# Kernel optimization log

Measured on AMD Instinct MI355X. Metric: run time of the kernel, lower is better.

## Reference

```python
import jax, jax.numpy as jnp
import numpy as np

B, NG, C, H = 16, 1024, 768, 12
CAP = 16  # fixed routing capacity in gpu_pair (8 box slots from 0 up, 8 cls slots from 15 down)


def layernorm(x, g, b, eps=1e-5):
    m = x.mean(-1, keepdims=True)
    v = jnp.mean((x - m) ** 2, axis=-1, keepdims=True)
    return (x - m) * jax.lax.rsqrt(v + eps) * g + b


def setup_inputs() -> dict:
    key = jax.random.key(0)
    ks = jax.random.split(key, 8)
    s = 0.02
    return {
        "general_token": jax.random.normal(ks[0], (B, NG, C), jnp.float32),
        "cls_token": jax.random.normal(ks[1], (B, 1, C), jnp.float32),
        "box_token": jax.random.normal(ks[2], (B, 1, C), jnp.float32),
        "w_qkv": jax.random.normal(ks[3], (3 * C, C), jnp.float32) * s,
        "w_proj": jax.random.normal(ks[4], (C, C), jnp.float32) * s,
        "b_proj": jnp.zeros((C,), jnp.float32),
        "gamma1": jnp.ones((C,), jnp.float32),
        "beta1": jnp.zeros((C,), jnp.float32),
    }


def _route(sum_a, is_box):
    """On-device replication of gpu_pair's serial CPU loop for slots 0..15.

    Tokens are processed in descending sum_attn order; box-preferred tokens fill
    slots 0,1,2,..., cls-preferred tokens fill slots 15,14,13,.... Each category's
    writer per slot is unique; on a box/cls collision the later (larger sorted
    position) write wins, matching the serial loop's overwrite semantics. Slots
    never written stay 0 (np.zeros init). Wrapped-around writes (rank >= 16) land
    outside slots 0..15 in the original and are irrelevant to the output.
    """
    ng = sum_a.shape[0]
    perm = jnp.argsort(-sum_a)                      # descending sort
    ib = is_box[perm]
    ibi = ib.astype(jnp.int32)
    box_rank = jnp.cumsum(ibi) - ibi                # exclusive prefix count of box tokens
    cls_rank = jnp.cumsum(1 - ibi) - (1 - ibi)      # exclusive prefix count of cls tokens
    j = jnp.arange(ng, dtype=jnp.int32)
    box_pos = jnp.where(ib & (box_rank < CAP), box_rank, CAP)
    cls_pos = jnp.where((~ib) & (cls_rank < CAP), (CAP - 1) - cls_rank, CAP)
    empty = jnp.full((CAP,), -1, jnp.int32)
    box_j = empty.at[box_pos].set(j, mode='drop')   # unique writer per slot
    cls_j = empty.at[cls_pos].set(j, mode='drop')
    win = jnp.maximum(box_j, cls_j)
    return jnp.where(win >= 0, perm[jnp.maximum(win, 0)], 0)


def reference(general_token, cls_token, box_token, w_qkv, w_proj, b_proj, gamma1, beta1):
    # cat order in torch: cat(cls, cat(box, general)) -> [cls, box, general]
    cat = jnp.concatenate([cls_token, box_token, general_token], axis=1)  # [B,N,C]
    Bq, N, Cq = cat.shape
    hd = Cq // H
    x = layernorm(cat, gamma1, beta1)
    qkv = (x @ w_qkv.T).reshape(Bq, N, 3, H, hd).transpose(2, 0, 3, 1, 4)
    q, k, v = qkv[0], qkv[1], qkv[2]
    attn = jnp.einsum('bhnd,bhmd->bhnm', q, k) * (hd ** -0.5)
    # raw scores between cls<->box zeroed BEFORE softmax (not -inf)
    attn = attn.at[:, :, 0, 1].set(0.0).at[:, :, 1, 0].set(0.0)
    attn = jax.nn.softmax(attn, axis=-1)
    out = jnp.einsum('bhnm,bhmd->bhnd', attn, v).transpose(0, 2, 1, 3).reshape(Bq, N, Cq)
    out = out @ w_proj.T + b_proj
    cat = cat + out  # residual (drop_path identity in eval)
    cls_t, box_t, gen = cat[:, 0:1], cat[:, 1:2], cat[:, 2:]
    cls_attn = attn[:, :, 0, 2:].mean(axis=1)  # [B, N-2]
    box_attn = attn[:, :, 1, 2:].mean(axis=1)
    idx = jax.vmap(_route)(cls_attn + box_attn, box_attn > cls_attn)  # [B,16]
    gathered = jnp.take_along_axis(gen, idx[:, :, None], axis=1)      # [B,16,C]
    cls_task_token = jnp.concatenate([cls_t, gathered[:, 0:8]], axis=1)   # [B,9,C]
    box_task_token = jnp.concatenate([box_t, gathered[:, 8:16]], axis=1)  # [B,9,C]
    return cls_task_token, box_task_token
```

## Files before the change

### kernel.cpp

```cpp
#include <hip/hip_runtime.h>
#include <math.h>

namespace {

constexpr int Bn = 16;
constexpr int NG = 1024;
constexpr int Cc = 768;
constexpr int Hh = 12;
constexpr int HD = 64;
constexpr int Nn = 1026;
constexpr int NR = 18;
constexpr int NPK = 1152;
constexpr int NCH = 16;

typedef __attribute__((ext_vector_type(8))) short short8;
typedef __attribute__((ext_vector_type(4))) float f32x4;

__device__ inline unsigned short f2bf(float f) {
  unsigned u = __float_as_uint(f);
  unsigned r = u + 0x7FFFu + ((u >> 16) & 1u);
  return (unsigned short)(r >> 16);
}

__global__ __launch_bounds__(256) void k_ln(
    const float* __restrict__ gen, const float* __restrict__ cls,
    const float* __restrict__ box, const float* __restrict__ gamma,
    const float* __restrict__ beta, float* __restrict__ x,
    unsigned short* __restrict__ xbf) {
  int blk = blockIdx.x;
  int t = threadIdx.x;
  if (blk >= Bn * Nn) {
    constexpr int PERB = (NPK - Nn) * Cc / 2;
    int idx = (blk - Bn * Nn) * 256 + t;
    int total = Bn * PERB;
    for (int i = idx; i < total; i += 96 * 256) {
      int b = i / PERB, r = i % PERB;
      unsigned int* p = (unsigned int*)(xbf + ((size_t)b * NPK + Nn) * Cc);
      p[r] = 0u;
    }
    return;
  }
  int b = blk / Nn, n = blk % Nn;
  const float* src = (n == 0) ? cls + (size_t)b * Cc
                   : (n == 1) ? box + (size_t)b * Cc
                              : gen + ((size_t)b * NG + (n - 2)) * Cc;
  float v0 = src[t], v1 = src[t + 256], v2 = src[t + 512];
  __shared__ double red[8];
  double s = (double)v0 + (double)v1 + (double)v2;
  for (int o = 32; o > 0; o >>= 1) s += __shfl_down(s, o, 64);
  int wid = t >> 6, lid = t & 63;
  if (lid == 0) red[wid] = s;
  __syncthreads();
  if (t == 0) red[4] = (red[0] + red[1] + red[2] + red[3]) / Cc;
  __syncthreads();
  double mean = red[4];
  double d0 = (double)v0 - mean, d1 = (double)v1 - mean, d2 = (double)v2 - mean;
  double sq = d0 * d0 + d1 * d1 + d2 * d2;
  for (int o = 32; o > 0; o >>= 1) sq += __shfl_down(sq, o, 64);
  __syncthreads();
  if (lid == 0) red[wid] = sq;
  __syncthreads();
  if (t == 0) {
    double var = (red[0] + red[1] + red[2] + red[3]) / Cc;
    red[5] = 1.0 / sqrt(var + 1e-5);
  }
  __syncthreads();
  double rs = red[5];
  float* dst = x + ((size_t)b * Nn + n) * Cc;
  unsigned short* dbf = xbf + ((size_t)b * NPK + n) * Cc;
  float o0 = (float)(d0 * rs * (double)gamma[t]       + (double)beta[t]);
  float o1 = (float)(d1 * rs * (double)gamma[t + 256] + (double)beta[t + 256]);
  float o2 = (float)(d2 * rs * (double)gamma[t + 512] + (double)beta[t + 512]);
  dst[t] = o0; dst[t + 256] = o1; dst[t + 512] = o2;
  dbf[t] = f2bf(o0); dbf[t + 256] = f2bf(o1); dbf[t + 512] = f2bf(o2);
}

__global__ __launch_bounds__(256) void k_mega1(
    const unsigned short* __restrict__ xbf, unsigned short* __restrict__ xT,
    const float* __restrict__ wqkv, const float* __restrict__ wproj,
    unsigned short* __restrict__ wqb, unsigned short* __restrict__ wvb,
    unsigned short* __restrict__ wpb, unsigned short* __restrict__ wkTb,
    const float* __restrict__ x, double* __restrict__ q01d) {
  __shared__ __align__(16) char smem[64 * 80 * 2];
  int blk = blockIdx.x;
  int t = threadIdx.x;
  if (blk < 3456) {
    int b = blk / 216, rem = blk % 216;
    int jt = rem / 12, ct = rem % 12;
    int j0 = jt * 64, c0 = ct * 64;
    auto ts = (unsigned short(*)[80])smem;
    #pragma unroll
    for (int l = 0; l < 2; l++) {
      int chunk = t + l * 256;
      int r = chunk >> 3, c8 = chunk & 7;
      uint4 v = *(const uint4*)(xbf + ((size_t)b * NPK + j0 + r) * Cc + c0 + c8 * 8);
      *(uint4*)&ts[r][c8 * 8] = v;
    }
    __syncthreads();
    #pragma unroll
    for (int l = 0; l < 2; l++) {
      int chunk = t + l * 256;
      int orow = chunk >> 3, j8 = chunk & 7;
      unsigned short tmp[8];
      #pragma unroll
      for (int i = 0; i < 8; i++) tmp[i] = ts[j8 * 8 + i][orow];
      *(uint4*)(xT + ((size_t)b * Cc + c0 + orow) * NPK + j0 + j8 * 8) = *(uint4*)tmp;
    }
  } else if (blk < 4032) {
    int i = ((blk - 3456) * 256 + t) * 4;
    const float* wq = wqkv;
    const float* wv = wqkv + (size_t)2 * Cc * Cc;
    float4 q = *(const float4*)(wq + i);
    float4 a = *(const float4*)(wv + i);
    float4 b = *(const float4*)(wproj + i);
    ushort4 oq, oa, ob;
    oq.x = f2bf(q.x); oq.y = f2bf(q.y); oq.z = f2bf(q.z); oq.w = f2bf(q.w);
    oa.x = f2bf(a.x); oa.y = f2bf(a.y); oa.z = f2bf(a.z); oa.w = f2bf(a.w);
    ob.x = f2bf(b.x); ob.y = f2bf(b.y); ob.z = f2bf(b.z); ob.w = f2bf(b.w);
    *(ushort4*)(wqb + i) = oq;
    *(ushort4*)(wvb + i) = oa;
    *(ushort4*)(wpb + i) = ob;
  } else if (blk < 4176) {
    int q = blk - 4032;
    int rt = q / 12, ct = q % 12;
    auto ts = (unsigned short(*)[72])smem;
    const float* src = wqkv + (size_t)Cc * Cc;
    #pragma unroll
    for (int l = 0; l < 4; l++) {
      int idx = t + l * 256;
      int r = idx >> 4, c4 = idx & 15;
      float4 v = *(const float4*)(src + (size_t)(rt * 64 + r) * Cc + ct * 64 + c4 * 4);
      ts[r][c4 * 4 + 0] = f2bf(v.x); ts[r][c4 * 4 + 1] = f2bf(v.y);
      ts[r][c4 * 4 + 2] = f2bf(v.z); ts[r][c4 * 4 + 3] = f2bf(v.w);
    }
    __syncthreads();
    #pragma unroll
    for (int l = 0; l < 2; l++) {
      int idx = t + l * 256;
      int r2 = idx >> 3, j8 = idx & 7;
      unsigned short tmp[8];
      #pragma unroll
      for (int i = 0; i < 8; i++) tmp[i] = ts[j8 * 8 + i][r2];
      *(uint4*)(wkTb + (size_t)(ct * 64 + r2) * Cc + rt * 64 + j8 * 8) = *(uint4*)tmp;
    }
  } else {
    int q = blk - 4176;
    int row = q & 31;
    int ot = q >> 5;
    int b = row >> 1, i = row & 1;
    float* xl = (float*)smem;
    const float* xr = x + ((size_t)b * Nn + i) * Cc;
    for (int c = t; c < Cc; c += 256) xl[c] = xr[c];
    __syncthreads();
    int w = t >> 6, lane = t & 63;
    int o = ot * 4 + w;
    const float* wr = wqkv + (size_t)o * Cc + lane * 12;
    const float* xs = xl + lane * 12;
    double acc = 0;
    #pragma unroll
    for (int k = 0; k < 12; k++) acc += (double)wr[k] * (double)xs[k];
    for (int off = 32; off > 0; off >>= 1) acc += __shfl_down(acc, off, 64);
    if (lane == 0) q01d[(size_t)row * Cc + o] = acc;
  }
}

__global__ __launch_bounds__(256) void k_u01(
    const float* __restrict__ wqkv, const double* __restrict__ q01d,
    double* __restrict__ u01d) {
  int blk = blockIdx.x;
  int h = blk % Hh; int i = (blk / Hh) & 1; int b = blk / (2 * Hh);
  __shared__ double qh[HD];
  const double* q = q01d + ((size_t)b * 2 + i) * Cc + h * HD;
  if (threadIdx.x < HD) qh[threadIdx.x] = q[threadIdx.x];
  __syncthreads();
  const float* wk = wqkv + (size_t)Cc * Cc;
  int c = blockIdx.y * 256 + threadIdx.x;
  double a0 = 0, a1 = 0, a2 = 0, a3 = 0;
  #pragma unroll 4
  for (int d = 0; d < HD; d += 4) {
    a0 += qh[d]     * (double)wk[(size_t)(h * HD + d) * Cc + c];
    a1 += qh[d + 1] * (double)wk[(size_t)(h * HD + d + 1) * Cc + c];
    a2 += qh[d + 2] * (double)wk[(size_t)(h * HD + d + 2) * Cc + c];
    a3 += qh[d + 3] * (double)wk[(size_t)(h * HD + d + 3) * Cc + c];
  }
  u01d[(((size_t)(b * 2 + i)) * Hh + h) * Cc + c] = (a0 + a1) + (a2 + a3);
}

__global__ __launch_bounds__(256) void k_mega2(
    const double* __restrict__ u01d, const float* __restrict__ x,
    float* __restrict__ Ldp, double* __restrict__ Ld01) {
  int blk = blockIdx.x;
  int t = threadIdx.x;
  if (blk >= 1024) {
    int q = blk - 1024;
    int b = q >> 1, i = q & 1;
    int w = t >> 6, lane = t & 63;
    for (int k = 0; k < 6; k++) {
      int p = w * 6 + k;
      int h = p >> 1, j = p & 1;
      const double* u = u01d + (((size_t)(b * 2 + i)) * Hh + h) * Cc;
      const float* xr = x + ((size_t)b * Nn + j) * Cc;
      double acc = 0;
      for (int c = lane; c < Cc; c += 64) acc += u[c] * (double)xr[c];
      for (int off = 32; off > 0; off >>= 1) acc += __shfl_down(acc, off, 64);
      if (lane == 0) Ld01[(((size_t)(b * 2 + i)) * Hh + h) * 2 + j] = acc * 0.125;
    }
    return;
  }
  int b = blk >> 6, jt = (blk >> 4) & 3, cch = blk & 15;
  int c0 = cch * 48;
  int w = t >> 6, lane = t & 63;
  int g = w >> 1;
  int hh = (w & 1) * 6;
  __shared__ double ut[24][48];
  __shared__ __align__(16) float xtT[16][260];
  for (int idx = t; idx < 24 * 48; idx += 256) {
    int row = idx / 48, cc = idx % 48;
    int ig = row / 12, hr = row % 12;
    ut[row][cc] = u01d[(((size_t)(b * 2 + ig)) * Hh + hr) * Cc + c0 + cc];
  }
  double acc[6][4] = {};
  for (int s = 0; s < 3; s++) {
    #pragma unroll
    for (int l = 0; l < 4; l++) {
      int idx = t + l * 256;
      int row = idx >> 2, c4 = idx & 3;
      const float* xr = x + ((size_t)b * Nn + 2 + jt * 256 + row) * Cc + c0 + s * 16 + c4 * 4;
      float4 v = *(const float4*)xr;
      xtT[c4 * 4 + 0][row] = v.x;
      xtT[c4 * 4 + 1][row] = v.y;
      xtT[c4 * 4 + 2][row] = v.z;
      xtT[c4 * 4 + 3][row] = v.w;
    }
    __syncthreads();
    for (int cc = 0; cc < 16; cc++) {
      float4 xa = *(const float4*)&xtT[cc][lane * 4];
      double x0 = (double)xa.x, x1 = (double)xa.y, x2 = (double)xa.z, x3 = (double)xa.w;
      #pragma unroll
      for (int r = 0; r < 6; r++) {
        double uv = ut[g * 12 + hh + r][s * 16 + cc];
        acc[r][0] += uv * x0; acc[r][1] += uv * x1;
        acc[r][2] += uv * x2; acc[r][3] += uv * x3;
      }
    }
    __syncthreads();
  }
  for (int r = 0; r < 6; r++) {
    int rowo = g * 12 + hh + r;
    float4 o0;
    o0.x = (float)(acc[r][0] * 0.125); o0.y = (float)(acc[r][1] * 0.125);
    o0.z = (float)(acc[r][2] * 0.125); o0.w = (float)(acc[r][3] * 0.125);
    size_t base = (((size_t)cch * Bn + b) * 24 + rowo) * 1024 + jt * 256 + lane * 4;
    *(float4*)&Ldp[base] = o0;
  }
}

__global__ __launch_bounds__(256) void k_rsoftmax(
    const float* __restrict__ Ldp, const double* __restrict__ Ld01,
    double* __restrict__ Ld, unsigned short* __restrict__ Pb) {
  int blk = blockIdx.x;
  int h = blk % Hh; int i = (blk / Hh) & 1; int b = blk / (2 * Hh);
  double* row = Ld + (size_t)blk * Nn;
  unsigned short* prow = Pb + ((size_t)b * 216 + i * Hh + h) * NPK;
  int t = threadIdx.x;
  size_t poff = ((size_t)b * 24 + i * 12 + h) * 1024;
  constexpr size_t PSTRIDE = (size_t)Bn * 24 * 1024;
  double lv[5];
  int cnt = 0;
  double mx = -1e300;
  for (int j = t; j < Nn; j += 256) {
    double L;
    if (j < 2) {
      L = Ld01[(((size_t)(b * 2 + i)) * Hh + h) * 2 + j];
      if (i == 0 && j == 1) L = 0.0;
      if (i == 1 && j == 0) L = 0.0;
    } else {
      L = 0;
      #pragma unroll
      for (int p = 0; p < NCH; p++) L += (double)Ldp[(size_t)p * PSTRIDE + poff + (j - 2)];
    }
    lv[cnt++] = L;
    mx = fmax(mx, L);
  }
  __shared__ double sd[256];
  sd[t] = mx; __syncthreads();
  for (int st = 128; st > 0; st >>= 1) { if (t < st) sd[t] = fmax(sd[t], sd[t + st]); __syncthreads(); }
  mx = sd[0]; __syncthreads();
  double sum = 0;
  for (int k = 0; k < cnt; k++) { lv[k] = exp(lv[k] - mx); sum += lv[k]; }
  sd[t] = sum; __syncthreads();
  for (int st = 128; st > 0; st >>= 1) { if (t < st) sd[t] += sd[t + st]; __syncthreads(); }
  double inv = 1.0 / sd[0];
  int k = 0;
  for (int j = t; j < Nn; j += 256) {
    double p = lv[k++] * inv;
    row[j] = p;
    prow[j] = f2bf((float)p);
  }
  for (int j = Nn + t; j < NPK; j += 256) prow[j] = 0;
}

__global__ __launch_bounds__(256) void k_rsroute(
    const double* __restrict__ Ld, int* __restrict__ rowcat) {
  int b = blockIdx.x, t = threadIdx.x;
  __shared__ double vals[NG];
  __shared__ unsigned char flags[NG];
  __shared__ double redv[4];
  __shared__ int redi[4];
  __shared__ int blist[16], clist[16];
  __shared__ double blv[16], clv[16];
  for (int jg = t; jg < NG; jg += 256) {
    int j = jg + 2;
    double cs = 0, bs = 0;
    for (int h = 0; h < Hh; h++) {
      cs += Ld[(((size_t)(b * 2 + 0)) * Hh + h) * Nn + j];
      bs += Ld[(((size_t)(b * 2 + 1)) * Hh + h) * Nn + j];
    }
    cs /= 12.0; bs /= 12.0;
    vals[jg] = cs + bs;
    flags[jg] = (bs - cs) > 0.0 ? 1 : 0;
  }
  __syncthreads();
  int half = t >> 7;
  int lt = t & 127;
  int wv = t >> 6;
  int lane = t & 63;
  for (int s = 0; s < 16; s++) {
    double bv = -1e300; int bi = 0x7fffffff;
    #pragma unroll
    for (int k = 0; k < 8; k++) {
      int j = lt * 8 + k;
      double v = vals[j];
      if (flags[j] == half && v > bv) { bv = v; bi = j; }
    }
    for (int off = 32; off > 0; off >>= 1) {
      double ov = __shfl_down(bv, off, 64);
      int oi = __shfl_down(bi, off, 64);
      if (ov > bv || (ov == bv && oi < bi)) { bv = ov; bi = oi; }
    }
    if (lane == 0) { redv[wv] = bv; redi[wv] = bi; }
    __syncthreads();
    if (lt == 0) {
      double v0 = redv[half * 2], v1 = redv[half * 2 + 1];
      int i0 = redi[half * 2], i1 = redi[half * 2 + 1];
      if (v1 > v0 || (v1 == v0 && i1 < i0)) { v0 = v1; i0 = i1; }
      int win = (v0 > -1e299) ? i0 : -1;
      if (half) { blist[s] = win; blv[s] = v0; }
      else      { clist[s] = win; clv[s] = v0; }
      if (win >= 0) vals[win] = -1e300;
    }
    __syncthreads();
  }
  if (t < 16) {
    int s = t;
    int bc = blist[s];
    int cl = clist[15 - s];
    double bvv = blv[s], cvv = clv[15 - s];
    int win;
    if (bc < 0 && cl < 0) win = -1;
    else if (bc < 0) win = cl;
    else if (cl < 0) win = bc;
    else {
      bool boxwins = (bvv < cvv) || (bvv == cvv && bc > cl);
      win = boxwins ? bc : cl;
    }
    int tok = (win >= 0) ? win : 0;
    rowcat[b * NR + 2 + s] = tok + 2;
  }
  if (t == 0) { rowcat[b * NR + 0] = 0; rowcat[b * NR + 1] = 1; }
}

__global__ __launch_bounds__(256) void k_qg_mfma(
    const unsigned short* __restrict__ xbf, const unsigned short* __restrict__ wqb,
    const int* __restrict__ rowcat, unsigned short* __restrict__ qb) {
  int mt = blockIdx.x, ng = blockIdx.y;
  int wid = threadIdx.x >> 6, lane = threadIdx.x & 63;
  int nt = ng * 4 + wid;
  int m = lane & 15, kg = lane >> 4;
  int rowi = mt * 16 + m;
  int b = rowi >> 4, s = rowi & 15;
  int tok = rowcat[b * NR + 2 + s];
  const unsigned short* abase = xbf + ((size_t)b * NPK + tok) * Cc + kg * 8;
  const unsigned short* bbase = wqb + (size_t)(nt * 16 + m) * Cc + kg * 8;
  f32x4 acc = {0, 0, 0, 0};
  for (int k0 = 0; k0 < Cc; k0 += 32) {
    short8 a = *(const short8*)(abase + k0);
    short8 bf = *(const short8*)(bbase + k0);
    acc = __builtin_amdgcn_mfma_f32_16x16x32_bf16(a, bf, acc, 0, 0, 0);
  }
  int c = nt * 16 + m;
  #pragma unroll
  for (int r = 0; r < 4; r++) {
    int rowo = mt * 16 + kg * 4 + r;
    qb[(size_t)rowo * Cc + c] = f2bf(acc[r]);
  }
}

__global__ __launch_bounds__(256) void k_ug_mfma(
    const unsigned short* __restrict__ qb, const unsigned short* __restrict__ wkTb,
    unsigned short* __restrict__ u16b) {
  int h = blockIdx.x, mt = blockIdx.y, ngz = blockIdx.z;
  int wid = threadIdx.x >> 6, lane = threadIdx.x & 63;
  int m = lane & 15, kg = lane >> 4;
  int rowi = mt * 16 + m;
  const unsigned short* abase = qb + (size_t)rowi * Cc + h * HD + kg * 8;
  f32x4 acc[4] = {{0,0,0,0},{0,0,0,0},{0,0,0,0},{0,0,0,0}};
  #pragma unroll
  for (int k0 = 0; k0 < HD; k0 += 32) {
    short8 a = *(const short8*)(abase + k0);
    #pragma unroll
    for (int t = 0; t < 4; t++) {
      int c = ngz * 256 + (wid * 4 + t) * 16 + m;
      short8 bf = *(const short8*)(wkTb + (size_t)c * Cc + h * HD + kg * 8 + k0);
      acc[t] = __builtin_amdgcn_mfma_f32_16x16x32_bf16(a, bf, acc[t], 0, 0, 0);
    }
  }
  #pragma unroll
  for (int t = 0; t < 4; t++) {
    int c = ngz * 256 + (wid * 4 + t) * 16 + m;
    #pragma unroll
    for (int r = 0; r < 4; r++) {
      int row = mt * 16 + kg * 4 + r;
      int b = row >> 4, s = row & 15;
      u16b[((size_t)b * 192 + s * Hh + h) * Cc + c] = f2bf(acc[t][r]);
    }
  }
}

__global__ __launch_bounds__(128) void k_glogits_mfma(
    const unsigned short* __restrict__ u16b, const unsigned short* __restrict__ xbf,
    float* __restrict__ S) {
  int b = blockIdx.x, mg = blockIdx.y, nz = blockIdx.z;
  __shared__ __align__(16) unsigned short Bs[2][128 * 32];
  int t = threadIdx.x, w = t >> 6, lane = t & 63;
  int m = lane & 15, kg = lane >> 4;
  const unsigned short* ap[4];
  #pragma unroll
  for (int mt = 0; mt < 4; mt++)
    ap[mt] = u16b + ((size_t)b * 192 + mg * 64 + mt * 16 + m) * Cc + kg * 8;
  const unsigned short* gB[4];
  int lofs[4];
  #pragma unroll
  for (int l = 0; l < 4; l++) {
    int chunk = l * 128 + t;
    int col = chunk >> 2, kq = chunk & 3;
    gB[l] = xbf + ((size_t)b * NPK + nz * 128 + col) * Cc + kq * 8;
    lofs[l] = col * 32 + kq * 8;
  }
  constexpr int NIT = Cc / 32;
  #pragma unroll
  for (int l = 0; l < 4; l++) *(short8*)&Bs[0][lofs[l]] = *(const short8*)gB[l];
  __syncthreads();
  f32x4 acc[4][4] = {};
  for (int it = 0; it < NIT; it++) {
    int k0 = it * 32;
    int cur = it & 1;
    short8 nx[4];
    if (it + 1 < NIT) {
      #pragma unroll
      for (int l = 0; l < 4; l++) nx[l] = *(const short8*)(gB[l] + k0 + 32);
    }
    short8 a[4];
    #pragma unroll
    for (int mt = 0; mt < 4; mt++) a[mt] = *(const short8*)(ap[mt] + k0);
    #pragma unroll
    for (int tt = 0; tt < 4; tt++) {
      int col = w * 64 + tt * 16 + m;
      short8 bf = *(const short8*)&Bs[cur][col * 32 + kg * 8];
      #pragma unroll
      for (int mt = 0; mt < 4; mt++)
        acc[mt][tt] = __builtin_amdgcn_mfma_f32_16x16x32_bf16(a[mt], bf, acc[mt][tt], 0, 0, 0);
    }
    if (it + 1 < NIT) {
      #pragma unroll
      for (int l = 0; l < 4; l++) *(short8*)&Bs[cur ^ 1][lofs[l]] = nx[l];
    }
    __syncthreads();
  }
  #pragma unroll
  for (int mt = 0; mt < 4; mt++) {
    #pragma unroll
    for (int tt = 0; tt < 4; tt++) {
      int col = nz * 128 + w * 64 + tt * 16 + m;
      #pragma unroll
      for (int r = 0; r < 4; r++) {
        int row = mg * 64 + mt * 16 + kg * 4 + r;
        S[((size_t)b * 192 + row) * NPK + col] = acc[mt][tt][r] * 0.125f;
      }
    }
  }
}

__global__ __launch_bounds__(256) void k_gsoftmax(
    const float* __restrict__ S, unsigned short* __restrict__ Pb) {
  int blk = blockIdx.x;
  int b = blk / 192, r = blk % 192;
  const float* row = S + ((size_t)b * 192 + r) * NPK;
  unsigned short* prow = Pb + ((size_t)b * 216 + 24 + r) * NPK;
  int t = threadIdx.x;
  __shared__ float sd[256];
  float mx = -1e30f;
  for (int j = t; j < Nn; j += 256) mx = fmaxf(mx, row[j]);
  sd[t] = mx; __syncthreads();
  for (int st = 128; st > 0; st >>= 1) { if (t < st) sd[t] = fmaxf(sd[t], sd[t + st]); __syncthreads(); }
  mx = sd[0]; __syncthreads();
  float sum = 0;
  for (int j = t; j < Nn; j += 256) sum += __expf(row[j] - mx);
  sd[t] = sum; __syncthreads();
  for (int st = 128; st > 0; st >>= 1) { if (t < st) sd[t] += sd[t + st]; __syncthreads(); }
  float inv = 1.0f / sd[0];
  for (int j = t; j < NPK; j += 256) {
    prow[j] = (j < Nn) ? f2bf(__expf(row[j] - mx) * inv) : (unsigned short)0;
  }
}

__global__ __launch_bounds__(128) void k_wsum_mfma(
    const unsigned short* __restrict__ Pb, const unsigned short* __restrict__ xT,
    unsigned short* __restrict__ wsumb) {
  int b = blockIdx.x, mg = blockIdx.y, nz = blockIdx.z;
  __shared__ __align__(16) unsigned short Bs[2][128 * 32];
  int t = threadIdx.x, w = t >> 6, lane = t & 63;
  int m = lane & 15, kg = lane >> 4;
  const unsigned short* ap[4];
  #pragma unroll
  for (int mt = 0; mt < 4; mt++) {
    int r = mg * 64 + mt * 16 + m;
    int rc = r < 216 ? r : 215;
    ap[mt] = Pb + ((size_t)b * 216 + rc) * NPK + kg * 8;
  }
  const unsigned short* gB[4];
  int lofs[4];
  #pragma unroll
  for (int l = 0; l < 4; l++) {
    int chunk = l * 128 + t;
    int col = chunk >> 2, kq = chunk & 3;
    gB[l] = xT + ((size_t)b * Cc + nz * 128 + col) * NPK + kq * 8;
    lofs[l] = col * 32 + kq * 8;
  }
  constexpr int NIT = NPK / 32;
  #pragma unroll
  for (int l = 0; l < 4; l++) *(short8*)&Bs[0][lofs[l]] = *(const short8*)gB[l];
  __syncthreads();
  f32x4 acc[4][4] = {};
  for (int it = 0; it < NIT; it++) {
    int k0 = it * 32;
    int cur = it & 1;
    short8 nx[4];
    if (it + 1 < NIT) {
      #pragma unroll
      for (int l = 0; l < 4; l++) nx[l] = *(const short8*)(gB[l] + k0 + 32);
    }
    short8 a[4];
    #pragma unroll
    for (int mt = 0; mt < 4; mt++) a[mt] = *(const short8*)(ap[mt] + k0);
    #pragma unroll
    for (int tt = 0; tt < 4; tt++) {
      int col = w * 64 + tt * 16 + m;
      short8 bf = *(const short8*)&Bs[cur][col * 32 + kg * 8];
      #pragma unroll
      for (int mt = 0; mt < 4; mt++)
        acc[mt][tt] = __builtin_amdgcn_mfma_f32_16x16x32_bf16(a[mt], bf, acc[mt][tt], 0, 0, 0);
    }
    if (it + 1 < NIT) {
      #pragma unroll
      for (int l = 0; l < 4; l++) *(short8*)&Bs[cur ^ 1][lofs[l]] = nx[l];
    }
    __syncthreads();
  }
  #pragma unroll
  for (int mt = 0; mt < 4; mt++) {
    #pragma unroll
    for (int tt = 0; tt < 4; tt++) {
      int col = nz * 128 + w * 64 + tt * 16 + m;
      #pragma unroll
      for (int r = 0; r < 4; r++) {
        int row = mg * 64 + mt * 16 + kg * 4 + r;
        if (row < 216) wsumb[((size_t)b * 216 + row) * Cc + col] = f2bf(acc[mt][tt][r]);
      }
    }
  }
}

__global__ __launch_bounds__(256) void k_attnout_mfma(
    const unsigned short* __restrict__ wsumb, const unsigned short* __restrict__ wvb,
    unsigned short* __restrict__ aob) {
  int h = blockIdx.x, mt = blockIdx.y;
  int wid = threadIdx.x >> 6, lane = threadIdx.x & 63;
  int m = lane & 15, kg = lane >> 4;
  int row = mt * 16 + m;
  int b = row / NR, i = row % NR;
  const unsigned short* abase = wsumb + ((size_t)b * 216 + i * 12 + h) * Cc + kg * 8;
  const unsigned short* bbase = wvb + (size_t)(h * HD + wid * 16 + m) * Cc + kg * 8;
  f32x4 acc = {0, 0, 0, 0};
  for (int k0 = 0; k0 < Cc; k0 += 32) {
    short8 a = *(const short8*)(abase + k0);
    short8 bf = *(const short8*)(bbase + k0);
    acc = __builtin_amdgcn_mfma_f32_16x16x32_bf16(a, bf, acc, 0, 0, 0);
  }
  #pragma unroll
  for (int r = 0; r < 4; r++) {
    int orow = mt * 16 + kg * 4 + r;
    int ocol = h * HD + wid * 16 + m;
    aob[(size_t)orow * Cc + ocol] = f2bf(acc[r]);
  }
}

__global__ __launch_bounds__(256) void k_proj_mfma(
    const unsigned short* __restrict__ aob, const unsigned short* __restrict__ wpb,
    const float* __restrict__ bproj, const int* __restrict__ rowcat,
    const float* __restrict__ gen, const float* __restrict__ cls,
    const float* __restrict__ box, float* __restrict__ out) {
  int mt = blockIdx.x, ng = blockIdx.y;
  int wid = threadIdx.x >> 6, lane = threadIdx.x & 63;
  int nt = ng * 4 + wid;
  int m = lane & 15, kg = lane >> 4;
  const unsigned short* abase = aob + (size_t)(mt * 16 + m) * Cc + kg * 8;
  const unsigned short* bbase = wpb + (size_t)(nt * 16 + m) * Cc + kg * 8;
  f32x4 acc = {0, 0, 0, 0};
  for (int k0 = 0; k0 < Cc; k0 += 32) {
    short8 a = *(const short8*)(abase + k0);
    short8 bf = *(const short8*)(bbase + k0);
    acc = __builtin_amdgcn_mfma_f32_16x16x32_bf16(a, bf, acc, 0, 0, 0);
  }
  int c = nt * 16 + m;
  float bp = bproj[c];
  #pragma unroll
  for (int r = 0; r < 4; r++) {
    int bi = mt * 16 + kg * 4 + r;
    int b = bi / NR, i = bi % NR;
    int tok = rowcat[b * NR + i];
    const float* src = (tok == 0) ? cls + (size_t)b * Cc
                     : (tok == 1) ? box + (size_t)b * Cc
                                  : gen + ((size_t)b * NG + tok - 2) * Cc;
    float val = acc[r] + bp + src[c];
    float* dst;
    if (i == 0)       dst = out + ((size_t)b * 9 + 0) * Cc;
    else if (i == 1)  dst = out + (size_t)Bn * 9 * Cc + ((size_t)b * 9 + 0) * Cc;
    else if (i < 10)  dst = out + ((size_t)b * 9 + (i - 1)) * Cc;
    else              dst = out + (size_t)Bn * 9 * Cc + ((size_t)b * 9 + (i - 9)) * Cc;
    dst[c] = val;
  }
}

}

extern "C" void kernel_launch(void* const* d_in, const int* in_sizes, int n_in,
                              void* d_out, int out_size, void* d_ws, size_t ws_size,
                              hipStream_t stream) {
  (void)in_sizes; (void)n_in; (void)out_size; (void)ws_size;
  const float* gen   = (const float*)d_in[0];
  const float* cls   = (const float*)d_in[1];
  const float* box   = (const float*)d_in[2];
  const float* wqkv  = (const float*)d_in[3];
  const float* wproj = (const float*)d_in[4];
  const float* bproj = (const float*)d_in[5];
  const float* gamma = (const float*)d_in[6];
  const float* beta  = (const float*)d_in[7];
  float* out = (float*)d_out;

  char* ws = (char*)d_ws;
  size_t off = 0;
  auto alloc = [&](size_t bytes) { void* p = ws + off; off += (bytes + 255) & ~(size_t)255; return p; };
  float* x             = (float*)alloc((size_t)Bn * Nn * Cc * 4);
  unsigned short* xbf  = (unsigned short*)alloc((size_t)Bn * NPK * Cc * 2);
  unsigned short* xT   = (unsigned short*)alloc((size_t)Bn * Cc * NPK * 2);
  unsigned short* qb   = (unsigned short*)alloc((size_t)256 * Cc * 2);
  unsigned short* u16b = (unsigned short*)alloc((size_t)Bn * 192 * Cc * 2);
  float* S             = (float*)alloc((size_t)Bn * 192 * NPK * 4);
  unsigned short* Pb   = (unsigned short*)alloc((size_t)Bn * 216 * NPK * 2);
  unsigned short* wsumb= (unsigned short*)alloc((size_t)Bn * 216 * Cc * 2);
  unsigned short* aob  = (unsigned short*)alloc((size_t)288 * Cc * 2);
  unsigned short* wqb  = (unsigned short*)alloc((size_t)Cc * Cc * 2);
  unsigned short* wvb  = (unsigned short*)alloc((size_t)Cc * Cc * 2);
  unsigned short* wpb  = (unsigned short*)alloc((size_t)Cc * Cc * 2);
  unsigned short* wkTb = (unsigned short*)alloc((size_t)Cc * Cc * 2);
  double* q01d         = (double*)alloc((size_t)Bn * 2 * Cc * 8);
  double* u01d         = (double*)alloc((size_t)Bn * 2 * Hh * Cc * 8);
  double* Ld           = (double*)alloc((size_t)Bn * 2 * Hh * Nn * 8);
  double* Ld01         = (double*)alloc((size_t)Bn * 2 * Hh * 2 * 8);
  float* Ldp           = (float*)alloc((size_t)NCH * Bn * 24 * 1024 * 4);
  int* rowcat          = (int*)alloc((size_t)Bn * NR * 4);

  k_ln<<<Bn * Nn + 96, 256, 0, stream>>>(gen, cls, box, gamma, beta, x, xbf);
  k_mega1<<<10320, 256, 0, stream>>>(xbf, xT, wqkv, wproj, wqb, wvb, wpb, wkTb, x, q01d);
  k_u01<<<dim3(Bn * 2 * Hh, 3), 256, 0, stream>>>(wqkv, q01d, u01d);
  k_mega2<<<1056, 256, 0, stream>>>(u01d, x, Ldp, Ld01);
  k_rsoftmax<<<Bn * 2 * Hh, 256, 0, stream>>>(Ldp, Ld01, Ld, Pb);
  k_rsroute<<<Bn, 256, 0, stream>>>(Ld, rowcat);
  k_qg_mfma<<<dim3(16, 12), 256, 0, stream>>>(xbf, wqb, rowcat, qb);
  k_ug_mfma<<<dim3(Hh, 16, 3), 256, 0, stream>>>(qb, wkTb, u16b);
  k_glogits_mfma<<<dim3(Bn, 3, 9), 128, 0, stream>>>(u16b, xbf, S);
  k_gsoftmax<<<Bn * 192, 256, 0, stream>>>(S, Pb);
  k_wsum_mfma<<<dim3(Bn, 4, 6), 128, 0, stream>>>(Pb, xT, wsumb);
  k_attnout_mfma<<<dim3(Hh, 18), 256, 0, stream>>>(wsumb, wvb, aob);
  k_proj_mfma<<<dim3(18, 12), 256, 0, stream>>>(aob, wpb, bproj, rowcat, gen, cls, box, out);
}
```

Measured before the change: 294.1 us.

## Store general-token logits in bf16, cache softmax values, split route head-sum

The general-token logits buffer S is now written as bf16 instead of fp32, which halves its traffic between the logits GEMM and the softmax. The softmax kernel keeps each thread's values in registers, so the row is read once instead of twice and exp is computed once. The per-head summation in the routing kernel moves into a separate 64-block kernel, so that reduction runs across more blocks and the serial route kernel only loads precomputed sums. Rounding logits to bf16 before softmax adds error, and there is one extra launch.

Measured after the change: 295.0 us. No clear change (+0.3%).

```diff
diff --git a/kernel.cpp b/kernel.cpp
--- a/kernel.cpp
+++ b/kernel.cpp
@@ -20,6 +20,9 @@
   unsigned u = __float_as_uint(f);
   unsigned r = u + 0x7FFFu + ((u >> 16) & 1u);
   return (unsigned short)(r >> 16);
+}
+__device__ inline float bf2f(unsigned short s) {
+  return __uint_as_float((unsigned)s << 16);
 }
 
 __global__ __launch_bounds__(256) void k_ln(
@@ -300,8 +303,25 @@
   for (int j = Nn + t; j < NPK; j += 256) prow[j] = 0;
 }
 
-__global__ __launch_bounds__(256) void k_rsroute(
-    const double* __restrict__ Ld, int* __restrict__ rowcat) {
+__global__ __launch_bounds__(256) void k_rsums(
+    const double* __restrict__ Ld, double* __restrict__ suma,
+    double* __restrict__ diffd) {
+  int b = blockIdx.x;
+  int jg = blockIdx.y * 256 + threadIdx.x;
+  int j = jg + 2;
+  double cs = 0, bs = 0;
+  for (int h = 0; h < Hh; h++) {
+    cs += Ld[(((size_t)(b * 2 + 0)) * Hh + h) * Nn + j];
+    bs += Ld[(((size_t)(b * 2 + 1)) * Hh + h) * Nn + j];
+  }
+  cs /= 12.0; bs /= 12.0;
+  suma[(size_t)b * NG + jg] = cs + bs;
+  diffd[(size_t)b * NG + jg] = bs - cs;
+}
+
+__global__ __launch_bounds__(256) void k_route(
+    const double* __restrict__ suma, const double* __restrict__ diffd,
+    int* __restrict__ rowcat) {
   int b = blockIdx.x, t = threadIdx.x;
   __shared__ double vals[NG];
   __shared__ unsigned char flags[NG];
@@ -309,16 +329,9 @@
   __shared__ int redi[4];
   __shared__ int blist[16], clist[16];
   __shared__ double blv[16], clv[16];
-  for (int jg = t; jg < NG; jg += 256) {
-    int j = jg + 2;
-    double cs = 0, bs = 0;
-    for (int h = 0; h < Hh; h++) {
-      cs += Ld[(((size_t)(b * 2 + 0)) * Hh + h) * Nn + j];
-      bs += Ld[(((size_t)(b * 2 + 1)) * Hh + h) * Nn + j];
-    }
-    cs /= 12.0; bs /= 12.0;
-    vals[jg] = cs + bs;
-    flags[jg] = (bs - cs) > 0.0 ? 1 : 0;
+  for (int j = t; j < NG; j += 256) {
+    vals[j] = suma[(size_t)b * NG + j];
+    flags[j] = diffd[(size_t)b * NG + j] > 0.0 ? 1 : 0;
   }
   __syncthreads();
   int half = t >> 7;
@@ -429,7 +442,7 @@
 
 __global__ __launch_bounds__(128) void k_glogits_mfma(
     const unsigned short* __restrict__ u16b, const unsigned short* __restrict__ xbf,
-    float* __restrict__ S) {
+    unsigned short* __restrict__ Sb) {
   int b = blockIdx.x, mg = blockIdx.y, nz = blockIdx.z;
   __shared__ __align__(16) unsigned short Bs[2][128 * 32];
   int t = threadIdx.x, w = t >> 6, lane = t & 63;
@@ -485,33 +498,39 @@
       #pragma unroll
       for (int r = 0; r < 4; r++) {
         int row = mg * 64 + mt * 16 + kg * 4 + r;
-        S[((size_t)b * 192 + row) * NPK + col] = acc[mt][tt][r] * 0.125f;
+        Sb[((size_t)b * 192 + row) * NPK + col] = f2bf(acc[mt][tt][r] * 0.125f);
       }
     }
   }
 }
 
 __global__ __launch_bounds__(256) void k_gsoftmax(
-    const float* __restrict__ S, unsigned short* __restrict__ Pb) {
+    const unsigned short* __restrict__ Sb, unsigned short* __restrict__ Pb) {
   int blk = blockIdx.x;
   int b = blk / 192, r = blk % 192;
-  const float* row = S + ((size_t)b * 192 + r) * NPK;
+  const unsigned short* row = Sb + ((size_t)b * 192 + r) * NPK;
   unsigned short* prow = Pb + ((size_t)b * 216 + 24 + r) * NPK;
   int t = threadIdx.x;
+  float lv[5];
+  int cnt = 0;
+  float mx = -1e30f;
+  for (int j = t; j < Nn; j += 256) {
+    float v = bf2f(row[j]);
+    lv[cnt++] = v;
+    mx = fmaxf(mx, v);
+  }
   __shared__ float sd[256];
-  float mx = -1e30f;
-  for (int j = t; j < Nn; j += 256) mx = fmaxf(mx, row[j]);
   sd[t] = mx; __syncthreads();
   for (int st = 128; st > 0; st >>= 1) { if (t < st) sd[t] = fmaxf(sd[t], sd[t + st]); __syncthreads(); }
   mx = sd[0]; __syncthreads();
   float sum = 0;
-  for (int j = t; j < Nn; j += 256) sum += __expf(row[j] - mx);
+  for (int k = 0; k < cnt; k++) { lv[k] = __expf(lv[k] - mx); sum += lv[k]; }
   sd[t] = sum; __syncthreads();
   for (int st = 128; st > 0; st >>= 1) { if (t < st) sd[t] += sd[t + st]; __syncthreads(); }
   float inv = 1.0f / sd[0];
-  for (int j = t; j < NPK; j += 256) {
-    prow[j] = (j < Nn) ? f2bf(__expf(row[j] - mx) * inv) : (unsigned short)0;
-  }
+  int k = 0;
+  for (int j = t; j < Nn; j += 256) prow[j] = f2bf(lv[k++] * inv);
+  for (int j = Nn + t; j < NPK; j += 256) prow[j] = 0;
 }
 
 __global__ __launch_bounds__(128) void k_wsum_mfma(
@@ -666,7 +685,7 @@
   unsigned short* xT   = (unsigned short*)alloc((size_t)Bn * Cc * NPK * 2);
   unsigned short* qb   = (unsigned short*)alloc((size_t)256 * Cc * 2);
   unsigned short* u16b = (unsigned short*)alloc((size_t)Bn * 192 * Cc * 2);
-  float* S             = (float*)alloc((size_t)Bn * 192 * NPK * 4);
+  unsigned short* Sb   = (unsigned short*)alloc((size_t)Bn * 192 * NPK * 2);
   unsigned short* Pb   = (unsigned short*)alloc((size_t)Bn * 216 * NPK * 2);
   unsigned short* wsumb= (unsigned short*)alloc((size_t)Bn * 216 * Cc * 2);
   unsigned short* aob  = (unsigned short*)alloc((size_t)288 * Cc * 2);
@@ -679,6 +698,8 @@
   double* Ld           = (double*)alloc((size_t)Bn * 2 * Hh * Nn * 8);
   double* Ld01         = (double*)alloc((size_t)Bn * 2 * Hh * 2 * 8);
   float* Ldp           = (float*)alloc((size_t)NCH * Bn * 24 * 1024 * 4);
+  double* suma         = (double*)alloc((size_t)Bn * NG * 8);
+  double* diffd        = (double*)alloc((size_t)Bn * NG * 8);
   int* rowcat          = (int*)alloc((size_t)Bn * NR * 4);
 
   k_ln<<<Bn * Nn + 96, 256, 0, stream>>>(gen, cls, box, gamma, beta, x, xbf);
@@ -686,11 +707,12 @@
   k_u01<<<dim3(Bn * 2 * Hh, 3), 256, 0, stream>>>(wqkv, q01d, u01d);
   k_mega2<<<1056, 256, 0, stream>>>(u01d, x, Ldp, Ld01);
   k_rsoftmax<<<Bn * 2 * Hh, 256, 0, stream>>>(Ldp, Ld01, Ld, Pb);
-  k_rsroute<<<Bn, 256, 0, stream>>>(Ld, rowcat);
+  k_rsums<<<dim3(Bn, 4), 256, 0, stream>>>(Ld, suma, diffd);
+  k_route<<<Bn, 256, 0, stream>>>(suma, diffd, rowcat);
   k_qg_mfma<<<dim3(16, 12), 256, 0, stream>>>(xbf, wqb, rowcat, qb);
   k_ug_mfma<<<dim3(Hh, 16, 3), 256, 0, stream>>>(qb, wkTb, u16b);
-  k_glogits_mfma<<<dim3(Bn, 3, 9), 128, 0, stream>>>(u16b, xbf, S);
-  k_gsoftmax<<<Bn * 192, 256, 0, stream>>>(S, Pb);
+  k_glogits_mfma<<<dim3(Bn, 3, 9), 128, 0, stream>>>(u16b, xbf, Sb);
+  k_gsoftmax<<<Bn * 192, 256, 0, stream>>>(Sb, Pb);
   k_wsum_mfma<<<dim3(Bn, 4, 6), 128, 0, stream>>>(Pb, xT, wsumb);
   k_attnout_mfma<<<dim3(Hh, 18), 256, 0, stream>>>(wsumb, wvb, aob);
   k_proj_mfma<<<dim3(18, 12), 256, 0, stream>>>(aob, wpb, bproj, rowcat, gen, cls, box, out);
```
